# Kernel optimization log

Measured on AMD Instinct MI355X. Metric: run time of the kernel, lower is better.

## Reference

```python
import jax, jax.numpy as jnp
import numpy as np

jax.config.update("jax_enable_x64", True)

# Dims (see shape_source): batch, heads, q-len, kv-len, head-channels, quant group
B, H, T, S, HC = 2, 16, 1024, 1024, 128
G = 8            # group_size from A/R_QUANT_PARAMS
SCALE_SHIFT = 14 # combined dequant shift applied to integer QK scores before softmax
O_SM = 14        # fixed-point offset of the integer softmax output (LUT-style)
PROB_QMAX = 255.0  # 8-bit unsigned probability mantissa (R_QUANT_PARAMS n_bits=8)


def _dequant_po2(q, s):
    """q: int mantissas [..., N], s: nonneg po2 shift exponents [..., N//G].
    Emulates (q << s) per group of G channels (pot_scale activation quantizer)."""
    s_full = jnp.repeat(s, G, axis=-1)
    return q.astype(jnp.float64) * jnp.exp2(s_full.astype(jnp.float64))


def setup_inputs() -> dict:
    key = jax.random.key(0)
    ks = jax.random.split(key, 6)
    # signed 8-bit mantissas in [-128, 127]
    q_q = jax.random.randint(ks[0], (B, H, T, HC), 0, 256, dtype=jnp.int32) - 128
    k_q = jax.random.randint(ks[1], (B, H, S, HC), 0, 256, dtype=jnp.int32) - 128
    vt_q = jax.random.randint(ks[2], (B, H, HC, S), 0, 256, dtype=jnp.int32) - 128
    # nonnegative power-of-two shifts, one per group of G=8
    q_s = jax.random.randint(ks[3], (B, H, T, HC // G), 0, 4, dtype=jnp.int32)
    k_s = jax.random.randint(ks[4], (B, H, S, HC // G), 0, 4, dtype=jnp.int32)
    vt_s = jax.random.randint(ks[5], (B, H, HC, S // G), 0, 4, dtype=jnp.int32)
    return {"q_q": q_q, "q_s": q_s, "k_q": k_q, "k_s": k_s, "vt_q": vt_q, "vt_s": vt_s}


def reference(q_q, q_s, k_q, k_s, vt_q, vt_s):
    # ---- shift_qk_matmul: (q_q << q_s) @ (k_q << k_s)^T in float64, truncated to int64
    q = _dequant_po2(q_q, q_s)                       # [B,H,T,HC] f64
    k = _dequant_po2(k_q, k_s)                       # [B,H,S,HC] f64
    scores = jnp.einsum("bhtc,bhsc->bhts", q, k).astype(jnp.int64)

    # ---- integer softmax emulation: rescale integer scores, softmax, then
    # re-quantize probabilities with an 8-bit per-group (G=8 along S) po2 scale
    logits = scores.astype(jnp.float32) * np.float32(2.0 ** (-SCALE_SHIFT) / np.sqrt(HC))
    p = jax.nn.softmax(logits, axis=-1)              # [B,H,T,S]
    val = jnp.round(p * (2.0 ** O_SM))               # fixed-point probs (ints)
    vg = val.reshape(B, H, T, S // G, G)
    gmax = jnp.max(vg, axis=-1, keepdims=True)
    r_shift = jnp.clip(jnp.ceil(jnp.log2(jnp.maximum(gmax, 1.0) / PROB_QMAX)), 0.0, None)
    r_q = jnp.clip(jnp.round(vg / jnp.exp2(r_shift)), 0.0, PROB_QMAX)
    r = (r_q * jnp.exp2(r_shift)).reshape(B, H, T, S).astype(jnp.float64)  # (r_q << r_s)

    # ---- shift_rv_matmul: r @ (vt_q << vt_s)^T in float64, truncated to int64
    vt = _dequant_po2(vt_q, vt_s)                    # [B,H,HC,S] f64
    a = jnp.einsum("bhts,bhcs->bhtc", r, vt).astype(jnp.int64)  # [B,H,T,HC]
    return a
```

## Files before the change

kernel.cpp:

```cpp
#include <hip/hip_runtime.h>
#include <string.h>


typedef int   v4i __attribute__((ext_vector_type(4)));
typedef float v4f __attribute__((ext_vector_type(4)));
typedef short v8s __attribute__((ext_vector_type(8)));
typedef unsigned v2u __attribute__((ext_vector_type(2)));

#define BHN 32
#define TN  1024
#define SN  1024
#define HCN 128
#define TT  16
#define KD_BH 262144
#define VD_BH 262144
#define WS_NEED ((size_t)BHN*(KD_BH+VD_BH))

__device__ __forceinline__ unsigned pack_b(int b0,int b1,int b2,int b3){
    return (unsigned)((b0&255)|((b1&255)<<8)|((b2&255)<<16)|((b3&255)<<24));
}

__device__ __forceinline__ void dig16(const int* __restrict__ p, int s0, int s1,
                                      v4i& hi, v4i& lo){
    #pragma unroll
    for (int wi=0; wi<4; ++wi){
        v4i m = *(const v4i*)(p + wi*4);
        int s = (wi<2) ? s0 : s1;
        int d0=m[0]<<s, d1=m[1]<<s, d2=m[2]<<s, d3=m[3]<<s;
        hi[wi] = (int)pack_b(d0>>4,d1>>4,d2>>4,d3>>4);
        lo[wi] = (int)pack_b(d0&15,d1&15,d2&15,d3&15);
    }
}

__device__ __forceinline__ unsigned short bf16_of_int(int v){
    return (unsigned short)(__float_as_uint((float)v) >> 16);
}

__global__ __launch_bounds__(256) void digitize(
    const int* __restrict__ k_q, const int* __restrict__ k_s,
    const int* __restrict__ vt_q, const int* __restrict__ vt_s,
    unsigned char* __restrict__ kd, unsigned char* __restrict__ vd)
{
    const int w    = threadIdx.x >> 6;
    const int lane = threadIdx.x & 63;
    const int l15  = lane & 15;
    const int task = blockIdx.x*4 + w;
    if (task < 4096){
        const int kc = task & 1, n = (task>>1)&7, ch = (task>>4)&7, bh = task>>7;
        const int q4   = lane >> 4;
        const int srow = bh*SN + ch*128 + n*16 + l15;
        const int gb   = srow*16 + kc*8 + q4*2;
        v4i hi, lo;
        dig16(k_q + (size_t)srow*HCN + kc*64 + q4*16, k_s[gb], k_s[gb+1], hi, lo);
        size_t base = (size_t)bh*KD_BH + (size_t)(ch*32768 + n*4096 + kc*2048 + lane*16);
        *(v4i*)(kd + base)        = hi;
        *(v4i*)(kd + base + 1024) = lo;
    } else {
        const int t  = task - 4096;
        const int n  = t & 7, kb = (t>>3)&31, bh = t>>8;
        const int sub = lane >> 4;
        const int row = bh*HCN + n*16 + l15;
        const int* vp = vt_q + (size_t)row*SN + kb*32 + sub*8;
        const int s   = vt_s[row*128 + kb*4 + sub];
        unsigned wds[4];
        #pragma unroll
        for (int j=0;j<4;j++){
            int a = vp[j*2]   << s;
            int b = vp[j*2+1] << s;
            wds[j] = (unsigned)bf16_of_int(a) | ((unsigned)bf16_of_int(b) << 16);
        }
        size_t base = (size_t)bh*VD_BH + (size_t)(((kb*8 + n)*64 + lane)*16);
        *(v4i*)(vd + base) = v4i{(int)wds[0],(int)wds[1],(int)wds[2],(int)wds[3]};
    }
}

template<bool PK>
__global__ __launch_bounds__(256,4) void mha_mfma(
    const int* __restrict__ q_q, const int* __restrict__ q_s,
    const int* __restrict__ k_q, const int* __restrict__ k_s,
    const int* __restrict__ vt_q, const int* __restrict__ vt_s,
    const unsigned char* __restrict__ kd, const unsigned char* __restrict__ vd,
    int* __restrict__ out)
{
    __shared__ __align__(16) unsigned short rbuf[16*1024];
    int*   redi = (int*)  (rbuf + 16128);
    float* redf = (float*)(rbuf + 16256);

    const int tid  = threadIdx.x;
    const int ln   = tid & 15;
    const int qd4  = (tid >> 4) & 3;
    const int w    = tid >> 6;
    const int lane = tid & 63;
    const int blk = blockIdx.x;
    const int bh  = ((blk>>9)<<3) | (blk&7);
    const int t0  = ((blk>>3)&63) * TT;

    v4i qfh[2], qfl[2];
    {
        const int* qrow  = q_q + (size_t)(bh*TN + t0 + ln)*HCN;
        const int* qsrow = q_s + (size_t)(bh*TN + t0 + ln)*16;
        #pragma unroll
        for (int kc=0; kc<2; ++kc){
            int gi = kc*8 + qd4*2;
            dig16(qrow + kc*64 + qd4*16, qsrow[gi], qsrow[gi+1], qfh[kc], qfl[kc]);
        }
    }

    int scv[16][4];

    const v4i* kb_ = (const v4i*)(kd + (size_t)bh*KD_BH);
    for (int ch=0; ch<8; ++ch){
        #pragma unroll
        for (int i=0;i<2;i++){
            const int n = w*2 + i;
            v4i a2{0,0,0,0}, a1{0,0,0,0}, a0{0,0,0,0};
            #pragma unroll
            for (int kc=0;kc<2;kc++){
                v4i bhv, blv;
                if (PK){
                    const v4i* tb = kb_ + (ch*8+n)*256 + kc*128 + lane;
                    bhv = tb[0];
                    blv = tb[64];
                } else {
                    int srow = bh*SN + ch*128 + n*16 + ln;
                    int cc   = kc*64 + qd4*16;
                    dig16(k_q + (size_t)srow*128 + cc,
                          k_s[srow*16 + (cc>>3)], k_s[srow*16 + (cc>>3) + 1], bhv, blv);
                }
                a2 = __builtin_amdgcn_mfma_i32_16x16x64_i8(bhv, qfh[kc], a2, 0,0,0);
                a1 = __builtin_amdgcn_mfma_i32_16x16x64_i8(bhv, qfl[kc], a1, 0,0,0);
                a1 = __builtin_amdgcn_mfma_i32_16x16x64_i8(blv, qfh[kc], a1, 0,0,0);
                a0 = __builtin_amdgcn_mfma_i32_16x16x64_i8(blv, qfl[kc], a0, 0,0,0);
            }
            int st = ch*2 + i;
            #pragma unroll
            for (int r=0;r<4;r++)
                scv[st][r] = (a2[r]<<8) + (a1[r]<<4) + a0[r];
        }
    }

    const float CS2 = (float)(6.103515625e-05 / 11.313708498984760390566
                              * 1.4426950408889634074);
    {
        int m0=-2147483647, m1=-2147483647, m2=-2147483647, m3=-2147483647;
        #pragma unroll
        for (int st=0;st<16;st++){
            m0 = max(m0, scv[st][0]);
            m1 = max(m1, scv[st][1]);
            m2 = max(m2, scv[st][2]);
            m3 = max(m3, scv[st][3]);
        }
        int m_ = max(max(m0,m1), max(m2,m3));
        m_ = max(m_, __shfl_xor(m_, 16));
        m_ = max(m_, __shfl_xor(m_, 32));
        if ((tid & 48) == 0) redi[w*16 + ln] = m_;
    }
    __syncthreads();
    float inv14;
    {
        const int mrow = max(max(redi[ln], redi[16+ln]), max(redi[32+ln], redi[48+ln]));
        float s0=0.f, s1=0.f, s2=0.f, s3=0.f;
        #pragma unroll
        for (int st=0;st<16;st++){
            #pragma unroll
            for (int r=0;r<4;r++){
                float t_ = (float)(scv[st][r] - mrow) * CS2;
                float e;
                asm("v_exp_f32 %0, %1" : "=v"(e) : "v"(t_));
                scv[st][r] = __float_as_int(e);
                if (r==0) s0 += e; else if (r==1) s1 += e; else if (r==2) s2 += e; else s3 += e;
            }
        }
        float s_ = (s0+s1) + (s2+s3);
        s_ += __shfl_xor(s_, 16);
        s_ += __shfl_xor(s_, 32);
        if ((tid & 48) == 0) redf[w*16 + ln] = s_;
    }
    __syncthreads();
    {
        float sum = redf[ln] + redf[16+ln] + redf[32+ln] + redf[48+ln];
        inv14 = 16384.0f / sum;
    }
    __syncthreads();

    {
        const int lnr4 = (ln & 7) << 4;
        const int cbase = w*32 + qd4*4;
        unsigned short* rp = rbuf + ln*1024;
        #pragma unroll
        for (int st=0;st<16;st++){
            float v0 = rintf(__int_as_float(scv[st][0]) * inv14);
            float v1 = rintf(__int_as_float(scv[st][1]) * inv14);
            float v2 = rintf(__int_as_float(scv[st][2]) * inv14);
            float v3 = rintf(__int_as_float(scv[st][3]) * inv14);
            float g = fmaxf(fmaxf(v0,v1), fmaxf(v2,v3));
            g = fmaxf(g, __shfl_xor(g, 16));
            int gi = max((int)g, 1);
            int x  = gi - 1;
            int e2 = 31 - __clz(x | 255);
            int sh = (e2 - 7) + ((x >> (e2 - 7)) == 255);
            float isc = __int_as_float((127 - sh) << 23);
            float fsc = __int_as_float((127 + sh) << 23);
            unsigned b0 = __float_as_uint(rintf(v0*isc) * fsc);
            unsigned b1 = __float_as_uint(rintf(v1*isc) * fsc);
            unsigned b2 = __float_as_uint(rintf(v2*isc) * fsc);
            unsigned b3 = __float_as_uint(rintf(v3*isc) * fsc);
            unsigned w0 = __builtin_amdgcn_perm(b1, b0, 0x07060302u);
            unsigned w1 = __builtin_amdgcn_perm(b3, b2, 0x07060302u);
            int c0 = (st>>1)*128 + cbase + (st&1)*16;
            *(v2u*)(rp + (c0 ^ lnr4)) = v2u{w0, w1};
        }
    }
    __syncthreads();

    const v4i* vb = (const v4i*)(vd + (size_t)bh*VD_BH);
    const unsigned short* rp2 = rbuf + ln*1024;
    const int lnr4b = (ln & 7) << 4;
    v4f acc0{0,0,0,0}, acc1{0,0,0,0};
    #pragma unroll 4
    for (int kb=0; kb<32; ++kb){
        v8s af = *(const v8s*)(rp2 + ((kb*32 + qd4*8) ^ lnr4b));
        v4i b0, b1;
        if (PK){
            b0 = vb[(kb*8 + w*2    )*64 + lane];
            b1 = vb[(kb*8 + w*2 + 1)*64 + lane];
        } else {
            #pragma unroll
            for (int i=0;i<2;i++){
                int chan = (w*2+i)*16 + ln;
                const int* vp = vt_q + (size_t)(bh*HCN + chan)*SN + kb*32 + qd4*8;
                int s = vt_s[(bh*HCN + chan)*128 + kb*4 + qd4];
                unsigned wd[4];
                #pragma unroll
                for (int j=0;j<4;j++){
                    int a = vp[j*2]   << s;
                    int b = vp[j*2+1] << s;
                    wd[j] = (unsigned)bf16_of_int(a) | ((unsigned)bf16_of_int(b)<<16);
                }
                v4i t{(int)wd[0],(int)wd[1],(int)wd[2],(int)wd[3]};
                if (i==0) b0 = t; else b1 = t;
            }
        }
        v8s bs0, bs1;
        memcpy(&bs0, &b0, 16);
        memcpy(&bs1, &b1, 16);
        acc0 = __builtin_amdgcn_mfma_f32_16x16x32_bf16(af, bs0, acc0, 0,0,0);
        acc1 = __builtin_amdgcn_mfma_f32_16x16x32_bf16(af, bs1, acc1, 0,0,0);
    }
    #pragma unroll
    for (int r=0;r<4;r++){
        size_t o = (size_t)(bh*TN + t0 + qd4*4 + r)*HCN + w*32 + ln;
        out[o]      = (int)rintf(acc0[r]);
        out[o + 16] = (int)rintf(acc1[r]);
    }
}

extern "C" void kernel_launch(void* const* d_in, const int* in_sizes, int n_in,
                              void* d_out, int out_size, void* d_ws, size_t ws_size,
                              hipStream_t stream) {
    const int* q_q  = (const int*)d_in[0];
    const int* q_s  = (const int*)d_in[1];
    const int* k_q  = (const int*)d_in[2];
    const int* k_s  = (const int*)d_in[3];
    const int* vt_q = (const int*)d_in[4];
    const int* vt_s = (const int*)d_in[5];
    int* out = (int*)d_out;

    unsigned char* kd = (unsigned char*)d_ws;
    unsigned char* vd = kd + (size_t)BHN*KD_BH;

    if (ws_size >= WS_NEED){
        digitize<<<dim3(3072), 256, 0, stream>>>(k_q,k_s,vt_q,vt_s, kd,vd);
        mha_mfma<true><<<dim3(2048), 256, 0, stream>>>(
            q_q,q_s,k_q,k_s,vt_q,vt_s, kd,vd, out);
    } else {
        mha_mfma<false><<<dim3(2048), 256, 0, stream>>>(
            q_q,q_s,k_q,k_s,vt_q,vt_s, kd,vd, out);
    }
}
```

Before: 152.1 us.

## Compute QK scores with bf16 MFMA instead of int8 nibble-split MFMAs

```diff
diff --git a/kernel.cpp b/kernel.cpp
--- a/kernel.cpp
+++ b/kernel.cpp
@@ -16,24 +16,19 @@
 #define VD_BH 262144
 #define WS_NEED ((size_t)BHN*(KD_BH+VD_BH))
 
-__device__ __forceinline__ unsigned pack_b(int b0,int b1,int b2,int b3){
-    return (unsigned)((b0&255)|((b1&255)<<8)|((b2&255)<<16)|((b3&255)<<24));
-}
-
-__device__ __forceinline__ void dig16(const int* __restrict__ p, int s0, int s1,
-                                      v4i& hi, v4i& lo){
-    #pragma unroll
-    for (int wi=0; wi<4; ++wi){
-        v4i m = *(const v4i*)(p + wi*4);
-        int s = (wi<2) ? s0 : s1;
-        int d0=m[0]<<s, d1=m[1]<<s, d2=m[2]<<s, d3=m[3]<<s;
-        hi[wi] = (int)pack_b(d0>>4,d1>>4,d2>>4,d3>>4);
-        lo[wi] = (int)pack_b(d0&15,d1&15,d2&15,d3&15);
-    }
-}
-
 __device__ __forceinline__ unsigned short bf16_of_int(int v){
     return (unsigned short)(__float_as_uint((float)v) >> 16);
+}
+
+__device__ __forceinline__ v4i pack8(const int* __restrict__ p, int s){
+    unsigned wd[4];
+    #pragma unroll
+    for (int j=0;j<4;j++){
+        int a = p[j*2]   << s;
+        int b = p[j*2+1] << s;
+        wd[j] = (unsigned)bf16_of_int(a) | ((unsigned)bf16_of_int(b) << 16);
+    }
+    return v4i{(int)wd[0],(int)wd[1],(int)wd[2],(int)wd[3]};
 }
 
 __global__ __launch_bounds__(256) void digitize(
@@ -44,33 +39,23 @@
     const int w    = threadIdx.x >> 6;
     const int lane = threadIdx.x & 63;
     const int l15  = lane & 15;
+    const int q4   = lane >> 4;
     const int task = blockIdx.x*4 + w;
-    if (task < 4096){
-        const int kc = task & 1, n = (task>>1)&7, ch = (task>>4)&7, bh = task>>7;
-        const int q4   = lane >> 4;
-        const int srow = bh*SN + ch*128 + n*16 + l15;
-        const int gb   = srow*16 + kc*8 + q4*2;
-        v4i hi, lo;
-        dig16(k_q + (size_t)srow*HCN + kc*64 + q4*16, k_s[gb], k_s[gb+1], hi, lo);
-        size_t base = (size_t)bh*KD_BH + (size_t)(ch*32768 + n*4096 + kc*2048 + lane*16);
-        *(v4i*)(kd + base)        = hi;
-        *(v4i*)(kd + base + 1024) = lo;
+    if (task < 8192){
+        const int kc = task & 3, n = (task>>2)&7, ch = (task>>5)&7, bh = task>>8;
+        const int row = bh*SN + ch*128 + n*16 + l15;
+        const int col = kc*32 + q4*8;
+        v4i f = pack8(k_q + (size_t)row*HCN + col, k_s[row*16 + (col>>3)]);
+        size_t base = (size_t)bh*KD_BH + (size_t)((((ch*8+n)*4 + kc)*64 + lane)*16);
+        *(v4i*)(kd + base) = f;
     } else {
-        const int t  = task - 4096;
+        const int t  = task - 8192;
         const int n  = t & 7, kb = (t>>3)&31, bh = t>>8;
-        const int sub = lane >> 4;
         const int row = bh*HCN + n*16 + l15;
-        const int* vp = vt_q + (size_t)row*SN + kb*32 + sub*8;
-        const int s   = vt_s[row*128 + kb*4 + sub];
-        unsigned wds[4];
-        #pragma unroll
-        for (int j=0;j<4;j++){
-            int a = vp[j*2]   << s;
-            int b = vp[j*2+1] << s;
-            wds[j] = (unsigned)bf16_of_int(a) | ((unsigned)bf16_of_int(b) << 16);
-        }
+        v4i f = pack8(vt_q + (size_t)row*SN + kb*32 + q4*8,
+                      vt_s[row*128 + kb*4 + q4]);
         size_t base = (size_t)bh*VD_BH + (size_t)(((kb*8 + n)*64 + lane)*16);
-        *(v4i*)(vd + base) = v4i{(int)wds[0],(int)wds[1],(int)wds[2],(int)wds[3]};
+        *(v4i*)(vd + base) = f;
     }
 }
 
@@ -83,7 +68,7 @@
     int* __restrict__ out)
 {
     __shared__ __align__(16) unsigned short rbuf[16*1024];
-    int*   redi = (int*)  (rbuf + 16128);
+    float* redm = (float*)(rbuf + 16128);
     float* redf = (float*)(rbuf + 16256);
 
     const int tid  = threadIdx.x;
@@ -95,79 +80,75 @@
     const int bh  = ((blk>>9)<<3) | (blk&7);
     const int t0  = ((blk>>3)&63) * TT;
 
-    v4i qfh[2], qfl[2];
-    {
-        const int* qrow  = q_q + (size_t)(bh*TN + t0 + ln)*HCN;
-        const int* qsrow = q_s + (size_t)(bh*TN + t0 + ln)*16;
-        #pragma unroll
-        for (int kc=0; kc<2; ++kc){
-            int gi = kc*8 + qd4*2;
-            dig16(qrow + kc*64 + qd4*16, qsrow[gi], qsrow[gi+1], qfh[kc], qfl[kc]);
-        }
-    }
-
-    int scv[16][4];
+    v8s qf[4];
+    {
+        const int* qrow = q_q + (size_t)(bh*TN + t0 + ln)*HCN;
+        const int* qs   = q_s + (size_t)(bh*TN + t0 + ln)*16;
+        #pragma unroll
+        for (int kc=0; kc<4; ++kc){
+            int col = kc*32 + qd4*8;
+            v4i t = pack8(qrow + col, qs[col>>3]);
+            memcpy(&qf[kc], &t, 16);
+        }
+    }
+
+    v4f scv[16];
 
     const v4i* kb_ = (const v4i*)(kd + (size_t)bh*KD_BH);
     for (int ch=0; ch<8; ++ch){
         #pragma unroll
         for (int i=0;i<2;i++){
             const int n = w*2 + i;
-            v4i a2{0,0,0,0}, a1{0,0,0,0}, a0{0,0,0,0};
+            v4f acc{0.f,0.f,0.f,0.f};
             #pragma unroll
-            for (int kc=0;kc<2;kc++){
-                v4i bhv, blv;
+            for (int kc=0;kc<4;kc++){
+                v8s af;
                 if (PK){
-                    const v4i* tb = kb_ + (ch*8+n)*256 + kc*128 + lane;
-                    bhv = tb[0];
-                    blv = tb[64];
+                    v4i a_ = kb_[((ch*8+n)*4 + kc)*64 + lane];
+                    memcpy(&af, &a_, 16);
                 } else {
                     int srow = bh*SN + ch*128 + n*16 + ln;
-                    int cc   = kc*64 + qd4*16;
-                    dig16(k_q + (size_t)srow*128 + cc,
-                          k_s[srow*16 + (cc>>3)], k_s[srow*16 + (cc>>3) + 1], bhv, blv);
+                    int cc   = kc*32 + qd4*8;
+                    v4i a_ = pack8(k_q + (size_t)srow*HCN + cc,
+                                   k_s[srow*16 + (cc>>3)]);
+                    memcpy(&af, &a_, 16);
                 }
-                a2 = __builtin_amdgcn_mfma_i32_16x16x64_i8(bhv, qfh[kc], a2, 0,0,0);
-                a1 = __builtin_amdgcn_mfma_i32_16x16x64_i8(bhv, qfl[kc], a1, 0,0,0);
-                a1 = __builtin_amdgcn_mfma_i32_16x16x64_i8(blv, qfh[kc], a1, 0,0,0);
-                a0 = __builtin_amdgcn_mfma_i32_16x16x64_i8(blv, qfl[kc], a0, 0,0,0);
+                acc = __builtin_amdgcn_mfma_f32_16x16x32_bf16(af, qf[kc], acc, 0,0,0);
             }
-            int st = ch*2 + i;
-            #pragma unroll
-            for (int r=0;r<4;r++)
-                scv[st][r] = (a2[r]<<8) + (a1[r]<<4) + a0[r];
+            scv[ch*2 + i] = acc;
         }
     }
 
     const float CS2 = (float)(6.103515625e-05 / 11.313708498984760390566
                               * 1.4426950408889634074);
     {
-        int m0=-2147483647, m1=-2147483647, m2=-2147483647, m3=-2147483647;
+        float m0=-3.0e38f, m1=-3.0e38f, m2=-3.0e38f, m3=-3.0e38f;
         #pragma unroll
         for (int st=0;st<16;st++){
-            m0 = max(m0, scv[st][0]);
-            m1 = max(m1, scv[st][1]);
-            m2 = max(m2, scv[st][2]);
-            m3 = max(m3, scv[st][3]);
-        }
-        int m_ = max(max(m0,m1), max(m2,m3));
-        m_ = max(m_, __shfl_xor(m_, 16));
-        m_ = max(m_, __shfl_xor(m_, 32));
-        if ((tid & 48) == 0) redi[w*16 + ln] = m_;
+            m0 = fmaxf(m0, scv[st][0]);
+            m1 = fmaxf(m1, scv[st][1]);
+            m2 = fmaxf(m2, scv[st][2]);
+            m3 = fmaxf(m3, scv[st][3]);
+        }
+        float m_ = fmaxf(fmaxf(m0,m1), fmaxf(m2,m3));
+        m_ = fmaxf(m_, __shfl_xor(m_, 16));
+        m_ = fmaxf(m_, __shfl_xor(m_, 32));
+        if ((tid & 48) == 0) redm[w*16 + ln] = m_;
     }
     __syncthreads();
     float inv14;
     {
-        const int mrow = max(max(redi[ln], redi[16+ln]), max(redi[32+ln], redi[48+ln]));
+        const float mrow = fmaxf(fmaxf(redm[ln], redm[16+ln]),
+                                 fmaxf(redm[32+ln], redm[48+ln]));
         float s0=0.f, s1=0.f, s2=0.f, s3=0.f;
         #pragma unroll
         for (int st=0;st<16;st++){
             #pragma unroll
             for (int r=0;r<4;r++){
-                float t_ = (float)(scv[st][r] - mrow) * CS2;
+                float t_ = (scv[st][r] - mrow) * CS2;
                 float e;
                 asm("v_exp_f32 %0, %1" : "=v"(e) : "v"(t_));
-                scv[st][r] = __float_as_int(e);
+                scv[st][r] = e;
                 if (r==0) s0 += e; else if (r==1) s1 += e; else if (r==2) s2 += e; else s3 += e;
             }
         }
@@ -189,10 +170,10 @@
         unsigned short* rp = rbuf + ln*1024;
         #pragma unroll
         for (int st=0;st<16;st++){
-            float v0 = rintf(__int_as_float(scv[st][0]) * inv14);
-            float v1 = rintf(__int_as_float(scv[st][1]) * inv14);
-            float v2 = rintf(__int_as_float(scv[st][2]) * inv14);
-            float v3 = rintf(__int_as_float(scv[st][3]) * inv14);
+            float v0 = rintf(scv[st][0] * inv14);
+            float v1 = rintf(scv[st][1] * inv14);
+            float v2 = rintf(scv[st][2] * inv14);
+            float v3 = rintf(scv[st][3] * inv14);
             float g = fmaxf(fmaxf(v0,v1), fmaxf(v2,v3));
             g = fmaxf(g, __shfl_xor(g, 16));
             int gi = max((int)g, 1);
@@ -228,16 +209,8 @@
             #pragma unroll
             for (int i=0;i<2;i++){
                 int chan = (w*2+i)*16 + ln;
-                const int* vp = vt_q + (size_t)(bh*HCN + chan)*SN + kb*32 + qd4*8;
-                int s = vt_s[(bh*HCN + chan)*128 + kb*4 + qd4];
-                unsigned wd[4];
-                #pragma unroll
-                for (int j=0;j<4;j++){
-                    int a = vp[j*2]   << s;
-                    int b = vp[j*2+1] << s;
-                    wd[j] = (unsigned)bf16_of_int(a) | ((unsigned)bf16_of_int(b)<<16);
-                }
-                v4i t{(int)wd[0],(int)wd[1],(int)wd[2],(int)wd[3]};
+                v4i t = pack8(vt_q + (size_t)(bh*HCN + chan)*SN + kb*32 + qd4*8,
+                              vt_s[(bh*HCN + chan)*128 + kb*4 + qd4]);
                 if (i==0) b0 = t; else b1 = t;
             }
         }
@@ -270,7 +243,7 @@
     unsigned char* vd = kd + (size_t)BHN*KD_BH;
 
     if (ws_size >= WS_NEED){
-        digitize<<<dim3(3072), 256, 0, stream>>>(k_q,k_s,vt_q,vt_s, kd,vd);
+        digitize<<<dim3(4096), 256, 0, stream>>>(k_q,k_s,vt_q,vt_s, kd,vd);
         mha_mfma<true><<<dim3(2048), 256, 0, stream>>>(
             q_q,q_s,k_q,k_s,vt_q,vt_s, kd,vd, out);
     } else {
```

Result: no change. 154.7 us (+1.7%).

## Double-buffer K and V fragment loads in registers and relax occupancy bound

Applied to the files above, without the earlier changes.

```diff
diff --git a/kernel.cpp b/kernel.cpp
--- a/kernel.cpp
+++ b/kernel.cpp
@@ -75,7 +75,7 @@
 }
 
 template<bool PK>
-__global__ __launch_bounds__(256,4) void mha_mfma(
+__global__ __launch_bounds__(256,3) void mha_mfma(
     const int* __restrict__ q_q, const int* __restrict__ q_s,
     const int* __restrict__ k_q, const int* __restrict__ k_s,
     const int* __restrict__ vt_q, const int* __restrict__ vt_s,
@@ -109,33 +109,57 @@
     int scv[16][4];
 
     const v4i* kb_ = (const v4i*)(kd + (size_t)bh*KD_BH);
-    for (int ch=0; ch<8; ++ch){
-        #pragma unroll
-        for (int i=0;i<2;i++){
-            const int n = w*2 + i;
+    if (PK){
+        v4i fb[2][4];
+        {
+            const v4i* ta = kb_ + (w*2)*256 + lane;
+            fb[0][0]=ta[0]; fb[0][1]=ta[64]; fb[0][2]=ta[128]; fb[0][3]=ta[192];
+        }
+        #pragma unroll
+        for (int t=0; t<16; ++t){
+            const int par = t & 1;
+            if (t < 15){
+                const int ch1 = (t+1)>>1, i1 = (t+1)&1;
+                const v4i* ta = kb_ + (ch1*8 + w*2 + i1)*256 + lane;
+                fb[par^1][0]=ta[0];   fb[par^1][1]=ta[64];
+                fb[par^1][2]=ta[128]; fb[par^1][3]=ta[192];
+            }
             v4i a2{0,0,0,0}, a1{0,0,0,0}, a0{0,0,0,0};
             #pragma unroll
             for (int kc=0;kc<2;kc++){
-                v4i bhv, blv;
-                if (PK){
-                    const v4i* tb = kb_ + (ch*8+n)*256 + kc*128 + lane;
-                    bhv = tb[0];
-                    blv = tb[64];
-                } else {
-                    int srow = bh*SN + ch*128 + n*16 + ln;
-                    int cc   = kc*64 + qd4*16;
-                    dig16(k_q + (size_t)srow*128 + cc,
-                          k_s[srow*16 + (cc>>3)], k_s[srow*16 + (cc>>3) + 1], bhv, blv);
-                }
+                v4i bhv = fb[par][kc*2], blv = fb[par][kc*2+1];
                 a2 = __builtin_amdgcn_mfma_i32_16x16x64_i8(bhv, qfh[kc], a2, 0,0,0);
                 a1 = __builtin_amdgcn_mfma_i32_16x16x64_i8(bhv, qfl[kc], a1, 0,0,0);
                 a1 = __builtin_amdgcn_mfma_i32_16x16x64_i8(blv, qfh[kc], a1, 0,0,0);
                 a0 = __builtin_amdgcn_mfma_i32_16x16x64_i8(blv, qfl[kc], a0, 0,0,0);
             }
-            int st = ch*2 + i;
             #pragma unroll
             for (int r=0;r<4;r++)
-                scv[st][r] = (a2[r]<<8) + (a1[r]<<4) + a0[r];
+                scv[t][r] = (a2[r]<<8) + (a1[r]<<4) + a0[r];
+        }
+    } else {
+        for (int ch=0; ch<8; ++ch){
+            #pragma unroll
+            for (int i=0;i<2;i++){
+                const int n = w*2 + i;
+                v4i a2{0,0,0,0}, a1{0,0,0,0}, a0{0,0,0,0};
+                #pragma unroll
+                for (int kc=0;kc<2;kc++){
+                    int srow = bh*SN + ch*128 + n*16 + ln;
+                    int cc   = kc*64 + qd4*16;
+                    v4i bhv, blv;
+                    dig16(k_q + (size_t)srow*128 + cc,
+                          k_s[srow*16 + (cc>>3)], k_s[srow*16 + (cc>>3) + 1], bhv, blv);
+                    a2 = __builtin_amdgcn_mfma_i32_16x16x64_i8(bhv, qfh[kc], a2, 0,0,0);
+                    a1 = __builtin_amdgcn_mfma_i32_16x16x64_i8(bhv, qfl[kc], a1, 0,0,0);
+                    a1 = __builtin_amdgcn_mfma_i32_16x16x64_i8(blv, qfh[kc], a1, 0,0,0);
+                    a0 = __builtin_amdgcn_mfma_i32_16x16x64_i8(blv, qfl[kc], a0, 0,0,0);
+                }
+                int st = ch*2 + i;
+                #pragma unroll
+                for (int r=0;r<4;r++)
+                    scv[st][r] = (a2[r]<<8) + (a1[r]<<4) + a0[r];
+            }
         }
     }
 
@@ -182,6 +206,17 @@
         inv14 = 16384.0f / sum;
     }
     __syncthreads();
+
+    const v4i* vb = (const v4i*)(vd + (size_t)bh*VD_BH);
+    v4i gb[2][8];
+    v8s ga[2][4];
+    if (PK){
+        #pragma unroll
+        for (int j=0;j<4;j++){
+            gb[0][j*2]   = vb[(j*8 + w*2    )*64 + lane];
+            gb[0][j*2+1] = vb[(j*8 + w*2 + 1)*64 + lane];
+        }
+    }
 
     {
         const int lnr4 = (ln & 7) << 4;
@@ -213,18 +248,39 @@
     }
     __syncthreads();
 
-    const v4i* vb = (const v4i*)(vd + (size_t)bh*VD_BH);
     const unsigned short* rp2 = rbuf + ln*1024;
     const int lnr4b = (ln & 7) << 4;
     v4f acc0{0,0,0,0}, acc1{0,0,0,0};
-    #pragma unroll 4
-    for (int kb=0; kb<32; ++kb){
-        v8s af = *(const v8s*)(rp2 + ((kb*32 + qd4*8) ^ lnr4b));
-        v4i b0, b1;
-        if (PK){
-            b0 = vb[(kb*8 + w*2    )*64 + lane];
-            b1 = vb[(kb*8 + w*2 + 1)*64 + lane];
-        } else {
+    if (PK){
+        #pragma unroll
+        for (int j=0;j<4;j++)
+            ga[0][j] = *(const v8s*)(rp2 + ((j*32 + qd4*8) ^ lnr4b));
+        #pragma unroll
+        for (int g=0; g<8; ++g){
+            const int par = g & 1;
+            if (g < 7){
+                #pragma unroll
+                for (int j=0;j<4;j++){
+                    int kb = (g+1)*4 + j;
+                    gb[par^1][j*2]   = vb[(kb*8 + w*2    )*64 + lane];
+                    gb[par^1][j*2+1] = vb[(kb*8 + w*2 + 1)*64 + lane];
+                    ga[par^1][j] = *(const v8s*)(rp2 + ((kb*32 + qd4*8) ^ lnr4b));
+                }
+            }
+            #pragma unroll
+            for (int j=0;j<4;j++){
+                v8s bs0, bs1;
+                memcpy(&bs0, &gb[par][j*2],   16);
+                memcpy(&bs1, &gb[par][j*2+1], 16);
+                acc0 = __builtin_amdgcn_mfma_f32_16x16x32_bf16(ga[par][j], bs0, acc0, 0,0,0);
+                acc1 = __builtin_amdgcn_mfma_f32_16x16x32_bf16(ga[par][j], bs1, acc1, 0,0,0);
+            }
+        }
+    } else {
+        #pragma unroll 4
+        for (int kb=0; kb<32; ++kb){
+            v8s af = *(const v8s*)(rp2 + ((kb*32 + qd4*8) ^ lnr4b));
+            v4i b0, b1;
             #pragma unroll
             for (int i=0;i<2;i++){
                 int chan = (w*2+i)*16 + ln;
@@ -240,12 +296,12 @@
                 v4i t{(int)wd[0],(int)wd[1],(int)wd[2],(int)wd[3]};
                 if (i==0) b0 = t; else b1 = t;
             }
-        }
-        v8s bs0, bs1;
-        memcpy(&bs0, &b0, 16);
-        memcpy(&bs1, &b1, 16);
-        acc0 = __builtin_amdgcn_mfma_f32_16x16x32_bf16(af, bs0, acc0, 0,0,0);
-        acc1 = __builtin_amdgcn_mfma_f32_16x16x32_bf16(af, bs1, acc1, 0,0,0);
+            v8s bs0, bs1;
+            memcpy(&bs0, &b0, 16);
+            memcpy(&bs1, &b1, 16);
+            acc0 = __builtin_amdgcn_mfma_f32_16x16x32_bf16(af, bs0, acc0, 0,0,0);
+            acc1 = __builtin_amdgcn_mfma_f32_16x16x32_bf16(af, bs1, acc1, 0,0,0);
+        }
     }
     #pragma unroll
     for (int r=0;r<4;r++){
```

Measured after the change: 150.7 us. About the same (-1.0%).
